# Kernel tuning notes

Measured on AMD Instinct MI355X. Metric: run time of the kernel, lower is better.

## Reference

```python
import jax, jax.numpy as jnp
import numpy as np

B, C, H, W = 32, 4, 512, 512
T = 64  # Angular_representive_Threshold
GROUPS = 2


def setup_inputs() -> dict:
    key = jax.random.key(0)
    k1, k2 = jax.random.split(key)
    x_real = jax.random.normal(k1, (B, C, H, W), dtype=jnp.float32)
    x_imag = jax.random.normal(k2, (B, C, H, W), dtype=jnp.float32)
    return {"x_real": x_real, "x_imag": x_imag}


def reference(x_real, x_imag):
    # Complex angular-delay input, split into 2 groups of 2 channels (torch.chunk dim=1)
    x = (x_real + 1j * x_imag).astype(jnp.complex64)            # [B,4,H,W]
    xg = x.reshape(B, GROUPS, 2, H, W)                          # [B,g,ch,H,W]
    ch0, ch1 = xg[:, :, 0], xg[:, :, 1]                         # [B,g,H,W]
    # sqrt(|real|^2) == |real|; energy difference summed over delay axis H (dim=2)
    diff = (jnp.abs(jnp.abs(ch0.real) - jnp.abs(ch1.imag)) +
            jnp.abs(jnp.abs(ch1.real) - jnp.abs(ch0.imag))).sum(axis=2)  # [B,g,W]
    # torch.sort ascending, keep first T indices (smallest energy difference)
    idx = jnp.argsort(diff, axis=-1)[..., :T]                   # [B,g,T]
    # vectorized column scatter replacing the per-batch/per-threshold python loops
    mask = jnp.zeros((B, GROUPS, W), jnp.float32).at[
        jnp.arange(B)[:, None, None],
        jnp.arange(GROUPS)[None, :, None],
        idx].set(1.0)                                           # [B,g,W]
    xm = xg * mask[:, :, None, None, :]                         # zero non-selected angular bins
    # ifft over delay (dim=-2) then fft over angle (dim=-1), +0.5 on real part
    out = jnp.fft.fft(jnp.fft.ifft(xm, axis=-2), axis=-1) + 0.5
    out = out.reshape(B, C, H, W).astype(jnp.complex64)         # concat of both groups on dim=1
    # return as stacked real/imag float32 (complex64 payload)
    return jnp.stack([out.real, out.imag], axis=-1)             # [B,4,H,W,2]
```

## Files before the change

### kernel.cpp

```cpp
#include <hip/hip_runtime.h>
#include <math.h>

#define NB 32
#define NC 4
#define NH 512
#define NW 512
#define NT 64
#define NG 2
#define BK 32

typedef __attribute__((ext_vector_type(8))) short short8;
typedef __attribute__((ext_vector_type(4))) float float4v;

__device__ inline unsigned short f2bf(float f) {
  union { float f; unsigned u; } v; v.f = f;
  unsigned r = v.u + 0x7FFF + ((v.u >> 16) & 1);
  return (unsigned short)(r >> 16);
}

__device__ __forceinline__ void gld16(const unsigned short* g, unsigned short* l) {
  __builtin_amdgcn_global_load_lds(
      (__attribute__((address_space(1))) const unsigned int*)g,
      (__attribute__((address_space(3))) unsigned int*)l, 16, 0, 0);
}

__global__ __launch_bounds__(256) void k_diff_t(const float* __restrict__ xr,
                                                const float* __restrict__ xi,
                                                float* __restrict__ diffp,
                                                unsigned short* __restrict__ Xt) {
  __shared__ __align__(16) unsigned short ldsA[512 * 40];
  __shared__ __align__(16) unsigned short ldsB[512 * 40];
  int bg = blockIdx.x, hc = blockIdx.y;
  int b = bg >> 1, g = bg & 1;
  int c0 = b * NC + 2 * g, c1 = c0 + 1;
  int t = threadIdx.x;
  int q = t & 127, rg = t >> 7;
  float4v acc = {0.f, 0.f, 0.f, 0.f};

#pragma unroll
  for (int phase = 0; phase < 2; ++phase) {
    const float* PA = (phase ? xr + (size_t)c1 * NH * NW : xr + (size_t)c0 * NH * NW);
    const float* PB = (phase ? xi + (size_t)c0 * NH * NW : xi + (size_t)c1 * NH * NW);
    int icA = phase ? c1 : c0;
    int icB = phase ? c0 : c1;
#pragma unroll
    for (int s = 0; s < 2; ++s) {
      int hbase = hc * 64 + s * 32 + rg * 16;
#pragma unroll
      for (int i8 = 0; i8 < 2; ++i8) {
        short8 pA[4], pB[4];
#pragma unroll
        for (int u = 0; u < 8; ++u) {
          int h = hbase + i8 * 8 + u;
          float4v a  = *(const float4v*)(PA + (size_t)h * NW + q * 4);
          float4v bb = *(const float4v*)(PB + (size_t)h * NW + q * 4);
#pragma unroll
          for (int k = 0; k < 4; ++k) {
            acc[k] += fabsf(fabsf(a[k]) - fabsf(bb[k]));
            pA[k][u] = (short)f2bf(a[k]);
            pB[k][u] = (short)f2bf(bb[k]);
          }
        }
        int ch = rg * 2 + i8;
#pragma unroll
        for (int k = 0; k < 4; ++k) {
          int w = q * 4 + k;
          int chs = ch ^ ((w >> 2) & 3);
          *(short8*)&ldsA[w * 40 + chs * 8] = pA[k];
          *(short8*)&ldsB[w * 40 + chs * 8] = pB[k];
        }
      }
      __syncthreads();
#pragma unroll
      for (int it = 0; it < 8; ++it) {
        int u = it * 256 + t;
        int w = u >> 2, cch = u & 3;
        int chs = cch ^ ((w >> 2) & 3);
        short8 vA = *(const short8*)&ldsA[w * 40 + chs * 8];
        short8 vB = *(const short8*)&ldsB[w * 40 + chs * 8];
        size_t colbase = (size_t)(hc * 64 + s * 32 + cch * 8);
        *(short8*)(Xt + ((size_t)(icA * 512 + w)) * 1024 + colbase)       = vA;
        *(short8*)(Xt + ((size_t)(icB * 512 + w)) * 1024 + 512 + colbase) = vB;
      }
      __syncthreads();
    }
  }

  float4v* red = (float4v*)ldsA;
  red[t] = acc;
  __syncthreads();
  if (t < 128) {
    float4v v = red[t];
    float4v u = red[t + 128];
#pragma unroll
    for (int k = 0; k < 4; ++k) v[k] += u[k];
    *(float4v*)(diffp + ((size_t)hc * 64 + bg) * NW + q * 4) = v;
  }
}

__global__ void k_select(const float* __restrict__ diffp, int* __restrict__ sel) {
  __shared__ float v[NW];
  int w = threadIdx.x;
  int bg = blockIdx.x;
  float mine = 0.f;
#pragma unroll
  for (int hc = 0; hc < 8; ++hc) mine += diffp[((size_t)hc * 64 + bg) * NW + w];
  v[w] = mine;
  __syncthreads();
  int rank = 0;
  for (int u = 0; u < NW; ++u) {
    float o = v[u];
    rank += (o < mine) || (o == mine && u < w);
  }
  if (rank < NT) sel[bg * NT + rank] = w;
}

__global__ __launch_bounds__(256) void k_build_T(unsigned short* __restrict__ Tb) {
  __shared__ float2 lt[512];
  int t = threadIdx.x;
  {
    float s, c;
    sincosf(6.2831853071795864769f * (float)t * (1.0f / 512.0f), &s, &c);
    lt[t] = make_float2(c, s);
    sincosf(6.2831853071795864769f * (float)(t + 256) * (1.0f / 512.0f), &s, &c);
    lt[t + 256] = make_float2(c, s);
  }
  __syncthreads();
  int idx0 = (blockIdx.x * 256 + t) * 8;
  int m = idx0 >> 10, k0 = idx0 & 1023;
  int hm = m & 511, rm = m >> 9;
  int rk = k0 >> 9;
  short8 o;
#pragma unroll
  for (int u = 0; u < 8; ++u) {
    int hk = (k0 + u) & 511;
    float2 cs = lt[(hm * hk) & 511];
    float val = (rm == rk) ? cs.x : (rk ? -cs.y : cs.y);
    o[u] = (short)f2bf(val * (1.0f / 512.0f));
  }
  *(short8*)(Tb + idx0) = o;
}

__global__ __launch_bounds__(256) void k_build_E(const int* __restrict__ sel,
                                                 unsigned short* __restrict__ Eb) {
  __shared__ int wsel[NT];
  __shared__ float2 lt[512];
  int bg = blockIdx.x;
  int t = threadIdx.x;
  {
    float s, c;
    sincosf(6.2831853071795864769f * (float)t * (1.0f / 512.0f), &s, &c);
    lt[t] = make_float2(c, s);
    sincosf(6.2831853071795864769f * (float)(t + 256) * (1.0f / 512.0f), &s, &c);
    lt[t + 256] = make_float2(c, s);
  }
  if (t < NT) wsel[t] = sel[bg * NT + t];
  __syncthreads();
  int base = blockIdx.y * 8192;
#pragma unroll
  for (int i = 0; i < 4; ++i) {
    int idx0 = base + (i * 256 + t) * 8;
    int n = idx0 >> 7, kidx0 = idx0 & 127;
    int j0 = kidx0 & 63, half = kidx0 >> 6;
    int part = n >> 9, kk = n & 511;
    short8 o;
#pragma unroll
    for (int u = 0; u < 8; ++u) {
      int w = wsel[j0 + u];
      float2 cs = lt[(kk * w) & 511];
      float val = part == 0 ? (half ? cs.y : cs.x) : (half ? cs.x : -cs.y);
      o[u] = (short)f2bf(val);
    }
    *(short8*)(Eb + (size_t)bg * 131072 + idx0) = o;
  }
}

__global__ __launch_bounds__(256) void k_gemm3(const unsigned short* __restrict__ Tb,
                                               const unsigned short* __restrict__ Xt,
                                               const int* __restrict__ sel,
                                               unsigned short* __restrict__ Yg) {
  __shared__ __align__(16) unsigned short Al[2][128 * BK];
  __shared__ __align__(16) unsigned short Bl[2][128 * BK];
  int lin = blockIdx.y * 64 + blockIdx.x;
  int swz = (lin & 7) * 64 + (lin >> 3);
  int n0 = (swz & 63) * 128;
  int m0 = (swz >> 6) * 128;
  int img0 = n0 >> 6;
  int bg = (img0 >> 2) * 2 + ((img0 >> 1) & 1);
  int tid = threadIdx.x;
  int lane = tid & 63, wid = tid >> 6;
  int wm = wid >> 1, wn = wid & 1;
  int quad = lane >> 4, l15 = lane & 15;
  int srow = lane >> 2, sqd = lane & 3;

  const unsigned short* srcA[2];
  const unsigned short* srcB[2];
#pragma unroll
  for (int p = 0; p < 2; ++p) {
    int chunk = wid * 2 + p;
    int row = chunk * 16 + srow;
    int sq = sqd ^ ((row >> 1) & 3);
    srcA[p] = Tb + (size_t)(m0 + row) * 1024 + sq * 8;
    int imgB = img0 + (row >> 6), j = row & 63;
    int w = sel[bg * NT + j];
    srcB[p] = Xt + ((size_t)(imgB * 512 + w)) * 1024 + sq * 8;
  }

  float4v acc[4][4];
#pragma unroll
  for (int i = 0; i < 4; ++i)
#pragma unroll
    for (int j = 0; j < 4; ++j) acc[i][j] = (float4v){0.f, 0.f, 0.f, 0.f};

#define STAGE3(buf, kk0)                                          \
  {                                                               \
    _Pragma("unroll")                                             \
    for (int p = 0; p < 2; ++p) {                                 \
      int chunk = wid * 2 + p;                                    \
      gld16(srcA[p] + (kk0), &Al[buf][chunk * 512]);              \
      gld16(srcB[p] + (kk0), &Bl[buf][chunk * 512]);              \
    }                                                             \
  }

  STAGE3(0, 0);
  __syncthreads();
  int cur = 0;
  for (int t = 0; t < 32; ++t) {
    if (t < 31) STAGE3(cur ^ 1, (t + 1) * 32);

    short8 af[4], bfv[4];
#pragma unroll
    for (int tt = 0; tt < 4; ++tt) {
      int ra = wm * 64 + tt * 16 + l15;
      int rb = wn * 64 + tt * 16 + l15;
      af[tt]  = *(const short8*)&Al[cur][ra * BK + ((quad ^ ((ra >> 1) & 3)) << 3)];
      bfv[tt] = *(const short8*)&Bl[cur][rb * BK + ((quad ^ ((rb >> 1) & 3)) << 3)];
    }
#pragma unroll
    for (int tm = 0; tm < 4; ++tm)
#pragma unroll
      for (int tn = 0; tn < 4; ++tn)
        acc[tm][tn] = __builtin_amdgcn_mfma_f32_16x16x32_bf16(af[tm], bfv[tn], acc[tm][tn], 0, 0, 0);

    __syncthreads();
    cur ^= 1;
  }

#pragma unroll
  for (int tm = 0; tm < 4; ++tm)
#pragma unroll
    for (int tn = 0; tn < 4; ++tn)
#pragma unroll
      for (int r = 0; r < 4; ++r) {
        int m = m0 + wm * 64 + tm * 16 + quad * 4 + r;
        int n = n0 + wn * 64 + tn * 16 + l15;
        int img = n >> 6, j = n & 63;
        int h = m & 511, ri = m >> 9;
        Yg[((size_t)img * 512 + h) * 128 + ri * 64 + j] = f2bf(acc[tm][tn][r]);
      }
}

__global__ __launch_bounds__(256) void k_gemm4(const unsigned short* __restrict__ Yg,
                                               const unsigned short* __restrict__ Eball,
                                               float2* __restrict__ out) {
  __shared__ __align__(16) unsigned short Al[128 * 128];
  __shared__ __align__(16) unsigned short Bl[128 * 128];
  int lin = blockIdx.x + blockIdx.y * 8 + blockIdx.z * 64;
  int swz = (lin & 7) * 512 + (lin >> 3);
  int n0 = (swz & 7) * 64;
  int m0 = ((swz >> 3) & 7) * 128;
  int bg = swz >> 6;
  int b = bg >> 1, g = bg & 1;
  int img0 = b * 4 + 2 * g;
  const unsigned short* Ab = Yg + (size_t)img0 * 512 * 128;
  const unsigned short* Eb = Eball + (size_t)bg * 131072;

  int tid = threadIdx.x;
  int lane = tid & 63, wid = tid >> 6;
  int wm = wid >> 1, wn = wid & 1;
  int quad = lane >> 4, l15 = lane & 15;
  int lrow4 = lane >> 4, cch = lane & 15;

#pragma unroll
  for (int c8 = 0; c8 < 8; ++c8) {
    int call = wid * 8 + c8;
    int row = call * 4 + lrow4;
    int sch = cch ^ (row & 7);
    gld16(&Ab[(size_t)(m0 + row) * 128 + sch * 8], &Al[call * 512]);
    int l = row & 63, wnB = row >> 6;
    int part = l >> 5;
    int grow = part * 512 + n0 + wnB * 32 + (l & 31);
    gld16(&Eb[(size_t)grow * 128 + sch * 8], &Bl[call * 512]);
  }
  __syncthreads();

  float4v acc[4][4];
#pragma unroll
  for (int i = 0; i < 4; ++i)
#pragma unroll
    for (int j = 0; j < 4; ++j) acc[i][j] = (float4v){0.f, 0.f, 0.f, 0.f};

#pragma unroll
  for (int ks = 0; ks < 4; ++ks) {
    short8 af[4], bfv[4];
#pragma unroll
    for (int tt = 0; tt < 4; ++tt) {
      int ra = wm * 64 + tt * 16 + l15;
      int rb = wn * 64 + tt * 16 + l15;
      af[tt]  = *(const short8*)&Al[ra * 128 + (((ks * 4 + quad) ^ (ra & 7)) << 3)];
      bfv[tt] = *(const short8*)&Bl[rb * 128 + (((ks * 4 + quad) ^ (rb & 7)) << 3)];
    }
#pragma unroll
    for (int tm = 0; tm < 4; ++tm)
#pragma unroll
      for (int tn = 0; tn < 4; ++tn)
        acc[tm][tn] = __builtin_amdgcn_mfma_f32_16x16x32_bf16(af[tm], bfv[tn], acc[tm][tn], 0, 0, 0);
  }

#pragma unroll
  for (int tm = 0; tm < 4; ++tm)
#pragma unroll
    for (int t2 = 0; t2 < 2; ++t2)
#pragma unroll
      for (int r = 0; r < 4; ++r) {
        int m = m0 + wm * 64 + tm * 16 + quad * 4 + r;
        int ch = m >> 9, h = m & 511;
        int img = img0 + ch;
        int kk = n0 + wn * 32 + t2 * 16 + l15;
        float2 v = make_float2(acc[tm][t2][r] + 0.5f, acc[tm][t2 + 2][r]);
        out[((size_t)(img * 512 + h)) * 512 + kk] = v;
      }
}

extern "C" void kernel_launch(void* const* d_in, const int* in_sizes, int n_in,
                              void* d_out, int out_size, void* d_ws, size_t ws_size,
                              hipStream_t stream) {
  const float* xr = (const float*)d_in[0];
  const float* xi = (const float*)d_in[1];
  float2* out = (float2*)d_out;

  char* ws = (char*)d_ws;
  float*          diffp = (float*)ws;
  int*            sel   = (int*)(ws + 1048576);
  unsigned short* Tb    = (unsigned short*)(ws + 2097152);
  unsigned short* Eb    = (unsigned short*)(ws + 4194304);
  unsigned short* Yg    = (unsigned short*)(ws + 20971520);
  unsigned short* Xt    = (unsigned short*)(ws + 37748736);

  k_diff_t <<<dim3(NB * NG, 8), 256, 0, stream>>>(xr, xi, diffp, Xt);
  k_select <<<NB * NG,          NW, 0, stream>>>(diffp, sel);
  k_build_T<<<512,              256, 0, stream>>>(Tb);
  k_build_E<<<dim3(NB * NG, 16),256, 0, stream>>>(sel, Eb);
  k_gemm3  <<<dim3(64, 8),      256, 0, stream>>>(Tb, Xt, sel, Yg);
  k_gemm4  <<<dim3(8, 8, 64),   256, 0, stream>>>(Yg, Eb, out);
}
```

Measured before the change: 572.0 us.

## Fold twiddle-matrix builds into diff and first GEMM kernels as extra blocks

The standalone kernels that build the bf16 DFT matrix T and the per-group E matrices are removed. T is now produced by extra blocks appended to the diff kernel's grid, and E by 64 extra blocks appended to the first GEMM kernel's grid. The aim is to cut two kernel launches and let the table builds overlap with the other work. In exchange, each E block now loops over 64 tiles serially instead of being spread across 16 blocks. The extra shared memory in the GEMM kernel may also reduce occupancy.

```diff
diff --git a/kernel.cpp b/kernel.cpp
--- a/kernel.cpp
+++ b/kernel.cpp
@@ -24,16 +24,45 @@
       (__attribute__((address_space(3))) unsigned int*)l, 16, 0, 0);
 }
 
-__global__ __launch_bounds__(256) void k_diff_t(const float* __restrict__ xr,
+__global__ __launch_bounds__(256) void k_diff_T(const float* __restrict__ xr,
                                                 const float* __restrict__ xi,
                                                 float* __restrict__ diffp,
-                                                unsigned short* __restrict__ Xt) {
+                                                unsigned short* __restrict__ Xt,
+                                                unsigned short* __restrict__ Tb) {
   __shared__ __align__(16) unsigned short ldsA[512 * 40];
   __shared__ __align__(16) unsigned short ldsB[512 * 40];
-  int bg = blockIdx.x, hc = blockIdx.y;
+  int lin = blockIdx.x;
+  int t = threadIdx.x;
+
+  if (lin >= 512) {
+    float2* lt = (float2*)ldsA;
+    {
+      float s, c;
+      sincosf(6.2831853071795864769f * (float)t * (1.0f / 512.0f), &s, &c);
+      lt[t] = make_float2(c, s);
+      sincosf(6.2831853071795864769f * (float)(t + 256) * (1.0f / 512.0f), &s, &c);
+      lt[t + 256] = make_float2(c, s);
+    }
+    __syncthreads();
+    int idx0 = ((lin - 512) * 256 + t) * 8;
+    int m = idx0 >> 10, k0 = idx0 & 1023;
+    int hm = m & 511, rm = m >> 9;
+    int rk = k0 >> 9;
+    short8 o;
+#pragma unroll
+    for (int u = 0; u < 8; ++u) {
+      int hk = (k0 + u) & 511;
+      float2 cs = lt[(hm * hk) & 511];
+      float val = (rm == rk) ? cs.x : (rk ? -cs.y : cs.y);
+      o[u] = (short)f2bf(val * (1.0f / 512.0f));
+    }
+    *(short8*)(Tb + idx0) = o;
+    return;
+  }
+
+  int bg = lin & 63, hc = lin >> 6;
   int b = bg >> 1, g = bg & 1;
   int c0 = b * NC + 2 * g, c1 = c0 + 1;
-  int t = threadIdx.x;
   int q = t & 127, rg = t >> 7;
   float4v acc = {0.f, 0.f, 0.f, 0.f};
 
@@ -115,79 +144,52 @@
   if (rank < NT) sel[bg * NT + rank] = w;
 }
 
-__global__ __launch_bounds__(256) void k_build_T(unsigned short* __restrict__ Tb) {
-  __shared__ float2 lt[512];
-  int t = threadIdx.x;
-  {
-    float s, c;
-    sincosf(6.2831853071795864769f * (float)t * (1.0f / 512.0f), &s, &c);
-    lt[t] = make_float2(c, s);
-    sincosf(6.2831853071795864769f * (float)(t + 256) * (1.0f / 512.0f), &s, &c);
-    lt[t + 256] = make_float2(c, s);
-  }
-  __syncthreads();
-  int idx0 = (blockIdx.x * 256 + t) * 8;
-  int m = idx0 >> 10, k0 = idx0 & 1023;
-  int hm = m & 511, rm = m >> 9;
-  int rk = k0 >> 9;
-  short8 o;
-#pragma unroll
-  for (int u = 0; u < 8; ++u) {
-    int hk = (k0 + u) & 511;
-    float2 cs = lt[(hm * hk) & 511];
-    float val = (rm == rk) ? cs.x : (rk ? -cs.y : cs.y);
-    o[u] = (short)f2bf(val * (1.0f / 512.0f));
-  }
-  *(short8*)(Tb + idx0) = o;
-}
-
-__global__ __launch_bounds__(256) void k_build_E(const int* __restrict__ sel,
-                                                 unsigned short* __restrict__ Eb) {
-  __shared__ int wsel[NT];
-  __shared__ float2 lt[512];
-  int bg = blockIdx.x;
-  int t = threadIdx.x;
-  {
-    float s, c;
-    sincosf(6.2831853071795864769f * (float)t * (1.0f / 512.0f), &s, &c);
-    lt[t] = make_float2(c, s);
-    sincosf(6.2831853071795864769f * (float)(t + 256) * (1.0f / 512.0f), &s, &c);
-    lt[t + 256] = make_float2(c, s);
-  }
-  if (t < NT) wsel[t] = sel[bg * NT + t];
-  __syncthreads();
-  int base = blockIdx.y * 8192;
-#pragma unroll
-  for (int i = 0; i < 4; ++i) {
-    int idx0 = base + (i * 256 + t) * 8;
-    int n = idx0 >> 7, kidx0 = idx0 & 127;
-    int j0 = kidx0 & 63, half = kidx0 >> 6;
-    int part = n >> 9, kk = n & 511;
-    short8 o;
-#pragma unroll
-    for (int u = 0; u < 8; ++u) {
-      int w = wsel[j0 + u];
-      float2 cs = lt[(kk * w) & 511];
-      float val = part == 0 ? (half ? cs.y : cs.x) : (half ? cs.x : -cs.y);
-      o[u] = (short)f2bf(val);
-    }
-    *(short8*)(Eb + (size_t)bg * 131072 + idx0) = o;
-  }
-}
-
-__global__ __launch_bounds__(256) void k_gemm3(const unsigned short* __restrict__ Tb,
-                                               const unsigned short* __restrict__ Xt,
-                                               const int* __restrict__ sel,
-                                               unsigned short* __restrict__ Yg) {
+__global__ __launch_bounds__(256) void k_gemm3E(const unsigned short* __restrict__ Tb,
+                                                const unsigned short* __restrict__ Xt,
+                                                const int* __restrict__ sel,
+                                                unsigned short* __restrict__ Yg,
+                                                unsigned short* __restrict__ Eb) {
   __shared__ __align__(16) unsigned short Al[2][128 * BK];
   __shared__ __align__(16) unsigned short Bl[2][128 * BK];
-  int lin = blockIdx.y * 64 + blockIdx.x;
+  __shared__ float2 ltE[512];
+  __shared__ int wselE[NT];
+  int lin = blockIdx.x;
+  int tid = threadIdx.x;
+
+  if (lin >= 512) {
+    int bg = lin - 512;
+    {
+      float s, c;
+      sincosf(6.2831853071795864769f * (float)tid * (1.0f / 512.0f), &s, &c);
+      ltE[tid] = make_float2(c, s);
+      sincosf(6.2831853071795864769f * (float)(tid + 256) * (1.0f / 512.0f), &s, &c);
+      ltE[tid + 256] = make_float2(c, s);
+    }
+    if (tid < NT) wselE[tid] = sel[bg * NT + tid];
+    __syncthreads();
+    for (int i = 0; i < 64; ++i) {
+      int idx0 = (i * 256 + tid) * 8;
+      int n = idx0 >> 7, kidx0 = idx0 & 127;
+      int j0 = kidx0 & 63, half = kidx0 >> 6;
+      int part = n >> 9, kk = n & 511;
+      short8 o;
+#pragma unroll
+      for (int u = 0; u < 8; ++u) {
+        int w = wselE[j0 + u];
+        float2 cs = ltE[(kk * w) & 511];
+        float val = part == 0 ? (half ? cs.y : cs.x) : (half ? cs.x : -cs.y);
+        o[u] = (short)f2bf(val);
+      }
+      *(short8*)(Eb + (size_t)bg * 131072 + idx0) = o;
+    }
+    return;
+  }
+
   int swz = (lin & 7) * 64 + (lin >> 3);
   int n0 = (swz & 63) * 128;
   int m0 = (swz >> 6) * 128;
   int img0 = n0 >> 6;
   int bg = (img0 >> 2) * 2 + ((img0 >> 1) & 1);
-  int tid = threadIdx.x;
   int lane = tid & 63, wid = tid >> 6;
   int wm = wid >> 1, wn = wid & 1;
   int quad = lane >> 4, l15 = lane & 15;
@@ -347,10 +349,8 @@
   unsigned short* Yg    = (unsigned short*)(ws + 20971520);
   unsigned short* Xt    = (unsigned short*)(ws + 37748736);
 
-  k_diff_t <<<dim3(NB * NG, 8), 256, 0, stream>>>(xr, xi, diffp, Xt);
-  k_select <<<NB * NG,          NW, 0, stream>>>(diffp, sel);
-  k_build_T<<<512,              256, 0, stream>>>(Tb);
-  k_build_E<<<dim3(NB * NG, 16),256, 0, stream>>>(sel, Eb);
-  k_gemm3  <<<dim3(64, 8),      256, 0, stream>>>(Tb, Xt, sel, Yg);
-  k_gemm4  <<<dim3(8, 8, 64),   256, 0, stream>>>(Yg, Eb, out);
-}
+  k_diff_T <<<1024,           256, 0, stream>>>(xr, xi, diffp, Xt, Tb);
+  k_select <<<NB * NG,        NW,  0, stream>>>(diffp, sel);
+  k_gemm3E <<<576,            256, 0, stream>>>(Tb, Xt, sel, Yg, Eb);
+  k_gemm4  <<<dim3(8, 8, 64), 256, 0, stream>>>(Yg, Eb, out);
+}
```

Measured after the change: 562.0 us. Within noise of the previous version (-1.7%).
